# Kernel tuning notes

Measured on AMD Instinct MI355X. Metric: run time of the kernel, lower is better.

## Reference

```python
import jax, jax.numpy as jnp
import numpy as np

N, E, D, L, R, G, C = 50000, 800000, 64, 3, 2, 128, 10


def setup_inputs() -> dict:
    key = jax.random.key(0)
    ks = jax.random.split(key, 16)
    s = 0.05
    x = jax.random.normal(ks[0], (N, D), dtype=jnp.float32)
    edge_index = jax.random.randint(ks[1], (2, E), 0, N, dtype=jnp.int64)
    edge_type = jax.random.randint(ks[2], (E,), 0, R, dtype=jnp.int64)
    batch = jnp.sort(jax.random.randint(ks[3], (N,), 0, G, dtype=jnp.int64))
    # per-layer self-loop Linear, per-(layer,relation) GIN eps + 2-layer MLP
    self_W = jax.random.normal(ks[4], (L, D, D), dtype=jnp.float32) * s
    self_b = jax.random.normal(ks[5], (L, D), dtype=jnp.float32) * s
    eps = jnp.zeros((L, R), dtype=jnp.float32)  # eps=0, train_eps=True
    mlp_W1 = jax.random.normal(ks[6], (L, R, D, D), dtype=jnp.float32) * s
    mlp_b1 = jax.random.normal(ks[7], (L, R, D), dtype=jnp.float32) * s
    mlp_W2 = jax.random.normal(ks[8], (L, R, D, D), dtype=jnp.float32) * s
    mlp_b2 = jax.random.normal(ks[9], (L, R, D), dtype=jnp.float32) * s
    lin1_W = jax.random.normal(ks[10], (D, D), dtype=jnp.float32) * s
    lin1_b = jax.random.normal(ks[11], (D,), dtype=jnp.float32) * s
    lin2_W = jax.random.normal(ks[12], (D, C), dtype=jnp.float32) * s
    lin2_b = jax.random.normal(ks[13], (C,), dtype=jnp.float32) * s
    return {"x": x, "edge_index": edge_index, "edge_type": edge_type, "batch": batch,
            "self_W": self_W, "self_b": self_b, "eps": eps,
            "mlp_W1": mlp_W1, "mlp_b1": mlp_b1, "mlp_W2": mlp_W2, "mlp_b2": mlp_b2,
            "lin1_W": lin1_W, "lin1_b": lin1_b, "lin2_W": lin2_W, "lin2_b": lin2_b}


def reference(x, edge_index, edge_type, batch, self_W, self_b, eps,
              mlp_W1, mlp_b1, mlp_W2, mlp_b2, lin1_W, lin1_b, lin2_W, lin2_b):
    src, dst = edge_index[0], edge_index[1]
    h = x
    for l in range(L):
        x_new = h @ self_W[l] + self_b[l]
        x_src = h[src]  # [E, D] gather of source features, done once per layer
        for r in range(R):
            # per-relation edge masking + scatter-add aggregation
            msg = jnp.where((edge_type == r)[:, None], x_src, jnp.zeros((), h.dtype))
            agg = jax.ops.segment_sum(msg, dst, num_segments=N)  # [N, D]
            z = (1.0 + eps[l, r]) * h + agg  # GIN combine
            z = jax.nn.relu(z @ mlp_W1[l, r] + mlp_b1[l, r])
            x_new = x_new + (z @ mlp_W2[l, r] + mlp_b2[l, r])
        h = x_new
    # global mean pooling over graphs
    sums = jax.ops.segment_sum(h, batch, num_segments=G)  # [G, D]
    counts = jax.ops.segment_sum(jnp.ones((N,), h.dtype), batch, num_segments=G)
    pooled = sums / jnp.maximum(counts, 1.0)[:, None]
    out = jax.nn.relu(pooled @ lin1_W + lin1_b)
    # dropout omitted (eval mode)
    out = out @ lin2_W + lin2_b
    return out
```

## Files before the change

kernel.cpp:

```cpp
#include <hip/hip_runtime.h>

#define Nn 50000
#define Dd 64
#define Ee 800000
#define Ll 3
#define Rr 2
#define Gg 128
#define Cc 10
#define NR (Nn * Rr)
#define NB ((NR + 1023) / 1024)
#define NT (Nn / 16)

#define CVT_B  3125
#define PREP_B 240
#define HIST_B 3125

typedef __attribute__((ext_vector_type(8))) short short8;
typedef __attribute__((ext_vector_type(4))) float f32x4;

__device__ __forceinline__ unsigned short bf16_rne(float x) {
  unsigned u = __float_as_uint(x);
  unsigned r = u + 0x7fffu + ((u >> 16) & 1u);
  return (unsigned short)(r >> 16);
}
__device__ __forceinline__ float bf16_tof(unsigned short b) {
  return __uint_as_float(((unsigned)b) << 16);
}
__device__ __forceinline__ void acc8(float* z, uint4 u) {
  z[0] += __uint_as_float(u.x << 16);
  z[1] += __uint_as_float(u.x & 0xffff0000u);
  z[2] += __uint_as_float(u.y << 16);
  z[3] += __uint_as_float(u.y & 0xffff0000u);
  z[4] += __uint_as_float(u.z << 16);
  z[5] += __uint_as_float(u.z & 0xffff0000u);
  z[6] += __uint_as_float(u.w << 16);
  z[7] += __uint_as_float(u.w & 0xffff0000u);
}

__global__ __launch_bounds__(256) void k_setup(
    const float* __restrict__ x, unsigned short* __restrict__ hb,
    const float* __restrict__ selfW, const float* __restrict__ W1,
    const float* __restrict__ W2, unsigned short* __restrict__ wtHi,
    unsigned short* __restrict__ wtLo,
    const int* __restrict__ dst, const int* __restrict__ et,
    int* __restrict__ counts)
{
  int b = blockIdx.x;
  if (b < CVT_B) {
    int i = b * 256 + threadIdx.x;
    const float4 v = *(const float4*)&x[(size_t)i * 4];
    ushort4 o;
    o.x = bf16_rne(v.x); o.y = bf16_rne(v.y);
    o.z = bf16_rne(v.z); o.w = bf16_rne(v.w);
    *(ushort4*)&hb[(size_t)i * 4] = o;
  } else if (b < CVT_B + PREP_B) {
    int i = (b - CVT_B) * 256 + threadIdx.x;
    int l = i / (5 * 4096);
    int rem = i - l * 5 * 4096;
    int m = rem >> 12;
    int e = rem & 4095;
    int k = e >> 6, c = e & 63;
    const float* p;
    if (m == 0)      p = selfW + (size_t)l * 4096;
    else if (m == 1) p = W1 + ((size_t)l * 2 + 0) * 4096;
    else if (m == 2) p = W2 + ((size_t)l * 2 + 0) * 4096;
    else if (m == 3) p = W1 + ((size_t)l * 2 + 1) * 4096;
    else             p = W2 + ((size_t)l * 2 + 1) * 4096;
    float w = p[e];
    unsigned short hi = bf16_rne(w);
    unsigned short lo = bf16_rne(w - bf16_tof(hi));
    size_t o = ((size_t)(l * 5 + m) * 64 + c) * 64 + k;
    wtHi[o] = hi;
    wtLo[o] = lo;
  } else {
    int e = (b - CVT_B - PREP_B) * 256 + threadIdx.x;
    atomicAdd(&counts[et[e] * Nn + dst[e]], 1);
  }
}

__global__ __launch_bounds__(1024) void k_scan1(
    const int* __restrict__ counts, int* __restrict__ offs,
    int* __restrict__ btot)
{
  __shared__ int s[1024];
  int i = blockIdx.x * 1024 + threadIdx.x;
  int v = (i < NR) ? counts[i] : 0;
  s[threadIdx.x] = v;
  __syncthreads();
#pragma unroll
  for (int d = 1; d < 1024; d <<= 1) {
    int t = (threadIdx.x >= d) ? s[threadIdx.x - d] : 0;
    __syncthreads();
    s[threadIdx.x] += t;
    __syncthreads();
  }
  if (i < NR) offs[i + 1] = s[threadIdx.x];
  if (threadIdx.x == 1023) btot[blockIdx.x] = s[1023];
}

__global__ __launch_bounds__(128) void k_scan2(
    const int* __restrict__ btot, int* __restrict__ bscan)
{
  __shared__ int s[128];
  int v = (threadIdx.x < NB) ? btot[threadIdx.x] : 0;
  s[threadIdx.x] = v;
  __syncthreads();
#pragma unroll
  for (int d = 1; d < 128; d <<= 1) {
    int t = (threadIdx.x >= d) ? s[threadIdx.x - d] : 0;
    __syncthreads();
    s[threadIdx.x] += t;
    __syncthreads();
  }
  if (threadIdx.x < NB) bscan[threadIdx.x] = s[threadIdx.x] - v;
}

__global__ __launch_bounds__(1024) void k_scan3(
    const int* __restrict__ counts, const int* __restrict__ bscan,
    int* __restrict__ offs, int* __restrict__ cursor)
{
  int i = blockIdx.x * 1024 + threadIdx.x;
  if (i >= NR) return;
  int o = offs[i + 1] + bscan[blockIdx.x];
  offs[i + 1] = o;
  cursor[i] = o - counts[i];
  if (i == 0) offs[0] = 0;
}

__global__ __launch_bounds__(256) void k_fill(
    const int* __restrict__ src, const int* __restrict__ dst,
    const int* __restrict__ et, int* __restrict__ cursor,
    int* __restrict__ elist)
{
  int e = blockIdx.x * 256 + threadIdx.x;
  if (e >= Ee) return;
  int pos = atomicAdd(&cursor[et[e] * Nn + dst[e]], 1);
  elist[pos] = src[e];
}

#define WOFF(m, c, ks) ((size_t)(m)*4096 + (size_t)(c)*64 + (ks)*32 + koff)

__global__ __launch_bounds__(128, 8) void k_update(
    const float* __restrict__ h, const unsigned short* __restrict__ hb,
    const int* __restrict__ offs, const int* __restrict__ elist,
    const unsigned short* __restrict__ wtHi, const unsigned short* __restrict__ wtLo,
    const float* __restrict__ selfb, const float* __restrict__ eps,
    const float* __restrict__ b1, const float* __restrict__ b2,
    float* __restrict__ hn, unsigned short* __restrict__ hnb, int l)
{
  __shared__ __align__(16) unsigned short tbh[2][16 * 72];
  __shared__ __align__(16) unsigned short tbl[2][16 * 72];
  float* xfer = (float*)&tbh[0][0];
  const int wave = threadIdx.x >> 6;
  const int lane = threadIdx.x & 63;
  const int task = blockIdx.x;
  const int r = wave;
  const int idx15 = lane & 15;
  const int kg = lane >> 4;
  const int koff = kg * 8;
  const int nodeA = task * 16 + idx15;

  float f[2][8];
  {
    const float* hp = &h[(size_t)nodeA * 64 + koff];
    const float4 a0 = *(const float4*)(hp);
    const float4 a1 = *(const float4*)(hp + 4);
    const float4 b0 = *(const float4*)(hp + 32);
    const float4 b1v = *(const float4*)(hp + 36);
    f[0][0] = a0.x; f[0][1] = a0.y; f[0][2] = a0.z; f[0][3] = a0.w;
    f[0][4] = a1.x; f[0][5] = a1.y; f[0][6] = a1.z; f[0][7] = a1.w;
    f[1][0] = b0.x; f[1][1] = b0.y; f[1][2] = b0.z; f[1][3] = b0.w;
    f[1][4] = b1v.x; f[1][5] = b1v.y; f[1][6] = b1v.z; f[1][7] = b1v.w;
  }

  const unsigned short* whi = wtHi + (size_t)l * 5 * 4096;
  const unsigned short* wlo = wtLo + (size_t)l * 5 * 4096;
  const int m1 = 1 + 2 * r, m2 = 2 + 2 * r;
  const float er = 1.0f + eps[l * Rr + r];

  float za[2][8];
#pragma unroll
  for (int ks = 0; ks < 2; ++ks)
#pragma unroll
    for (int j = 0; j < 8; ++j) za[ks][j] = 0.0f;
  {
    int aidx = r * Nn + nodeA;
    int jb = offs[aidx], je = offs[aidx + 1];
    int j = jb;
    for (; j + 3 < je; j += 4) {
      int s0 = elist[j], s1 = elist[j + 1], s2 = elist[j + 2], s3 = elist[j + 3];
      const unsigned short* q0 = &hb[(size_t)s0 * 64 + koff];
      const unsigned short* q1 = &hb[(size_t)s1 * 64 + koff];
      const unsigned short* q2 = &hb[(size_t)s2 * 64 + koff];
      const unsigned short* q3 = &hb[(size_t)s3 * 64 + koff];
      const uint4 a0 = *(const uint4*)(q0);
      const uint4 a1 = *(const uint4*)(q1);
      const uint4 a2 = *(const uint4*)(q2);
      const uint4 a3 = *(const uint4*)(q3);
      const uint4 b0 = *(const uint4*)(q0 + 32);
      const uint4 b1q = *(const uint4*)(q1 + 32);
      const uint4 b2q = *(const uint4*)(q2 + 32);
      const uint4 b3 = *(const uint4*)(q3 + 32);
      acc8(za[0], a0); acc8(za[0], a1); acc8(za[0], a2); acc8(za[0], a3);
      acc8(za[1], b0); acc8(za[1], b1q); acc8(za[1], b2q); acc8(za[1], b3);
    }
    for (; j < je; ++j) {
      const unsigned short* q = &hb[(size_t)elist[j] * 64 + koff];
      const uint4 a = *(const uint4*)(q);
      const uint4 b = *(const uint4*)(q + 32);
      acc8(za[0], a); acc8(za[1], b);
    }
  }

  short8 zhi[2], zlo[2];
#pragma unroll
  for (int ks = 0; ks < 2; ++ks)
#pragma unroll
    for (int j = 0; j < 8; ++j) {
      float zf = er * f[ks][j] + za[ks][j];
      unsigned short hb2 = bf16_rne(zf);
      zhi[ks][j] = (short)hb2;
      zlo[ks][j] = (short)bf16_rne(zf - bf16_tof(hb2));
    }

  f32x4 tacc[4];
#pragma unroll
  for (int cb = 0; cb < 4; ++cb) {
    float bi = b1[((size_t)l * 2 + r) * 64 + cb * 16 + idx15];
    tacc[cb] = (f32x4){bi, bi, bi, bi};
  }
#pragma unroll
  for (int cb = 0; cb < 4; ++cb) {
    int c = cb * 16 + idx15;
#pragma unroll
    for (int ks = 0; ks < 2; ++ks) {
      const short8 bh = *(const short8*)&whi[WOFF(m1, c, ks)];
      const short8 bl = *(const short8*)&wlo[WOFF(m1, c, ks)];
      tacc[cb] = __builtin_amdgcn_mfma_f32_16x16x32_bf16(zhi[ks], bh, tacc[cb], 0, 0, 0);
      tacc[cb] = __builtin_amdgcn_mfma_f32_16x16x32_bf16(zhi[ks], bl, tacc[cb], 0, 0, 0);
      tacc[cb] = __builtin_amdgcn_mfma_f32_16x16x32_bf16(zlo[ks], bh, tacc[cb], 0, 0, 0);
    }
  }
#pragma unroll
  for (int cb = 0; cb < 4; ++cb)
#pragma unroll
    for (int q = 0; q < 4; ++q) {
      float tv = fmaxf(tacc[cb][q], 0.0f);
      unsigned short hb2 = bf16_rne(tv);
      tbh[wave][(kg * 4 + q) * 72 + cb * 16 + idx15] = hb2;
      tbl[wave][(kg * 4 + q) * 72 + cb * 16 + idx15] = bf16_rne(tv - bf16_tof(hb2));
    }
  asm volatile("s_waitcnt lgkmcnt(0)" ::: "memory");
  __builtin_amdgcn_sched_barrier(0);
  short8 thi[2], tlo[2];
#pragma unroll
  for (int ks = 0; ks < 2; ++ks) {
    thi[ks] = *(const short8*)&tbh[wave][idx15 * 72 + ks * 32 + koff];
    tlo[ks] = *(const short8*)&tbl[wave][idx15 * 72 + ks * 32 + koff];
  }

  f32x4 facc[4];
#pragma unroll
  for (int cb = 0; cb < 4; ++cb) {
    int c = cb * 16 + idx15;
    float bi = b2[((size_t)l * 2 + r) * 64 + c];
    if (wave == 1) bi += selfb[l * 64 + c];
    facc[cb] = (f32x4){bi, bi, bi, bi};
  }
#pragma unroll
  for (int cb = 0; cb < 4; ++cb) {
    int c = cb * 16 + idx15;
#pragma unroll
    for (int ks = 0; ks < 2; ++ks) {
      const short8 bh = *(const short8*)&whi[WOFF(m2, c, ks)];
      const short8 bl = *(const short8*)&wlo[WOFF(m2, c, ks)];
      facc[cb] = __builtin_amdgcn_mfma_f32_16x16x32_bf16(thi[ks], bh, facc[cb], 0, 0, 0);
      facc[cb] = __builtin_amdgcn_mfma_f32_16x16x32_bf16(thi[ks], bl, facc[cb], 0, 0, 0);
      facc[cb] = __builtin_amdgcn_mfma_f32_16x16x32_bf16(tlo[ks], bh, facc[cb], 0, 0, 0);
    }
  }
  if (wave == 1) {
    short8 ahi[2], alo[2];
#pragma unroll
    for (int ks = 0; ks < 2; ++ks)
#pragma unroll
      for (int j = 0; j < 8; ++j) {
        unsigned short hb2 = bf16_rne(f[ks][j]);
        ahi[ks][j] = (short)hb2;
        alo[ks][j] = (short)bf16_rne(f[ks][j] - bf16_tof(hb2));
      }
#pragma unroll
    for (int cb = 0; cb < 4; ++cb) {
      int c = cb * 16 + idx15;
#pragma unroll
      for (int ks = 0; ks < 2; ++ks) {
        const short8 bh = *(const short8*)&whi[WOFF(0, c, ks)];
        const short8 bl = *(const short8*)&wlo[WOFF(0, c, ks)];
        facc[cb] = __builtin_amdgcn_mfma_f32_16x16x32_bf16(ahi[ks], bh, facc[cb], 0, 0, 0);
        facc[cb] = __builtin_amdgcn_mfma_f32_16x16x32_bf16(ahi[ks], bl, facc[cb], 0, 0, 0);
        facc[cb] = __builtin_amdgcn_mfma_f32_16x16x32_bf16(alo[ks], bh, facc[cb], 0, 0, 0);
      }
    }
  }
  __syncthreads();
  if (wave == 1) {
#pragma unroll
    for (int cb = 0; cb < 4; ++cb)
#pragma unroll
      for (int q = 0; q < 4; ++q)
        xfer[(kg * 4 + q) * 65 + cb * 16 + idx15] = facc[cb][q];
  }
  __syncthreads();
  if (wave == 0) {
#pragma unroll
    for (int cb = 0; cb < 4; ++cb)
#pragma unroll
      for (int q = 0; q < 4; ++q) {
        int row = kg * 4 + q, col = cb * 16 + idx15;
        float v = facc[cb][q] + xfer[row * 65 + col];
        size_t o = ((size_t)task * 16 + row) * 64 + col;
        hn[o] = v;
        hnb[o] = bf16_rne(v);
      }
  }
}

__global__ __launch_bounds__(64) void k_poolhead(
    const float* __restrict__ h, const int* __restrict__ batch,
    const float* __restrict__ l1W, const float* __restrict__ l1b,
    const float* __restrict__ l2W, const float* __restrict__ l2b,
    float* __restrict__ out)
{
  int g = blockIdx.x;
  int lane = threadIdx.x;
  int lo = 0, hi = Nn;
  while (lo < hi) { int mid = (lo + hi) >> 1; if (batch[mid] < g) lo = mid + 1; else hi = mid; }
  int start = lo;
  hi = Nn;
  while (lo < hi) { int mid = (lo + hi) >> 1; if (batch[mid] < g + 1) lo = mid + 1; else hi = mid; }
  int end = lo;

  float acc = 0.0f;
  int i = start;
  for (; i + 3 < end; i += 4) {
    float v0 = h[(size_t)i * 64 + lane];
    float v1 = h[(size_t)(i + 1) * 64 + lane];
    float v2 = h[(size_t)(i + 2) * 64 + lane];
    float v3 = h[(size_t)(i + 3) * 64 + lane];
    acc += (v0 + v1) + (v2 + v3);
  }
  for (; i < end; ++i) acc += h[(size_t)i * 64 + lane];
  float p = acc / fmaxf((float)(end - start), 1.0f);

  float t = l1b[lane];
#pragma unroll
  for (int k = 0; k < Dd; ++k)
    t += __shfl(p, k, 64) * l1W[k * Dd + lane];
  t = fmaxf(t, 0.0f);
  float o = (lane < Cc) ? l2b[lane] : 0.0f;
#pragma unroll
  for (int k = 0; k < Dd; ++k) {
    float w = (lane < Cc) ? l2W[k * Cc + lane] : 0.0f;
    o += __shfl(t, k, 64) * w;
  }
  if (lane < Cc) out[(size_t)g * Cc + lane] = o;
}

extern "C" void kernel_launch(void* const* d_in, const int* in_sizes, int n_in,
                              void* d_out, int out_size, void* d_ws, size_t ws_size,
                              hipStream_t stream)
{
  const float* x     = (const float*)d_in[0];
  const int*   ei    = (const int*)d_in[1];
  const int*   et    = (const int*)d_in[2];
  const int*   batch = (const int*)d_in[3];
  const float* selfW = (const float*)d_in[4];
  const float* selfb = (const float*)d_in[5];
  const float* eps   = (const float*)d_in[6];
  const float* W1    = (const float*)d_in[7];
  const float* b1    = (const float*)d_in[8];
  const float* W2    = (const float*)d_in[9];
  const float* b2    = (const float*)d_in[10];
  const float* l1W   = (const float*)d_in[11];
  const float* l1b   = (const float*)d_in[12];
  const float* l2W   = (const float*)d_in[13];
  const float* l2b   = (const float*)d_in[14];
  float* out = (float*)d_out;

  float* buf0 = (float*)d_ws;
  float* buf1 = buf0 + (size_t)Nn * Dd;
  unsigned short* hb0 = (unsigned short*)(buf1 + (size_t)Nn * Dd);
  unsigned short* hb1 = hb0 + (size_t)Nn * Dd;
  unsigned short* wtHi = hb1 + (size_t)Nn * Dd;
  unsigned short* wtLo = wtHi + (size_t)Ll * 5 * 4096;
  int* counts = (int*)(wtLo + (size_t)Ll * 5 * 4096);
  int* offs   = counts + NR;
  int* cursor = offs + NR + 1;
  int* btot   = cursor + NR;
  int* bscan  = btot + NB;
  int* elist  = bscan + NB;

  const int* src = ei;
  const int* dst = ei + Ee;

  hipMemsetAsync(counts, 0, (size_t)NR * sizeof(int), stream);
  k_setup<<<CVT_B + PREP_B + HIST_B, 256, 0, stream>>>(
      x, hb0, selfW, W1, W2, wtHi, wtLo, dst, et, counts);

  k_scan1<<<NB, 1024, 0, stream>>>(counts, offs, btot);
  k_scan2<<<1, 128, 0, stream>>>(btot, bscan);
  k_scan3<<<NB, 1024, 0, stream>>>(counts, bscan, offs, cursor);
  k_fill<<<(Ee + 255) / 256, 256, 0, stream>>>(src, dst, et, cursor, elist);

  const float* h = x;
  const unsigned short* hbc = hb0;
  float* hn = buf0;
  unsigned short* hnb = hb1;
  for (int l = 0; l < Ll; ++l) {
    k_update<<<NT, 128, 0, stream>>>(h, hbc, offs, elist, wtHi, wtLo,
                                     selfb, eps, b1, b2, hn, hnb, l);
    h = hn;
    hbc = hnb;
    hn = (hn == buf0) ? buf1 : buf0;
    hnb = (hnb == hb0) ? hb1 : hb0;
  }
  k_poolhead<<<Gg, 64, 0, stream>>>(h, batch, l1W, l1b, l2W, l2b, out);
}
```

Before: 335.2 us.

## Sort nodes by total in-degree so update tiles share similar edge counts

Adds a counting sort of nodes by total in-degree (capped at 127), producing a permutation that the CSR scan, fill and update kernels use. Each 16-node MFMA tile then groups nodes with similar neighbour counts, which reduces lane divergence in the gather loop. Output rows are written back through the permutation, so stores become scattered rather than contiguous. The occupancy hint on the update kernel is also lowered from 8 to 5 blocks, and three small preprocessing launches are added.

Result: slower. 451.8 us (+34.8%).

```diff
diff --git a/kernel.cpp b/kernel.cpp
--- a/kernel.cpp
+++ b/kernel.cpp
@@ -78,13 +78,62 @@
   }
 }
 
+__global__ __launch_bounds__(256) void k_deghist(
+    const int* __restrict__ counts, int* __restrict__ binh)
+{
+  __shared__ int lh[128];
+  if (threadIdx.x < 128) lh[threadIdx.x] = 0;
+  __syncthreads();
+  int n = blockIdx.x * 256 + threadIdx.x;
+  if (n < Nn) {
+    int t = min(counts[n] + counts[Nn + n], 127);
+    atomicAdd(&lh[t], 1);
+  }
+  __syncthreads();
+  if (threadIdx.x < 128 && lh[threadIdx.x] > 0)
+    atomicAdd(&binh[threadIdx.x], lh[threadIdx.x]);
+}
+
+__global__ __launch_bounds__(128) void k_binscan(
+    const int* __restrict__ binh, int* __restrict__ bincur)
+{
+  __shared__ int s[128];
+  int v = binh[threadIdx.x];
+  s[threadIdx.x] = v;
+  __syncthreads();
+#pragma unroll
+  for (int d = 1; d < 128; d <<= 1) {
+    int t = (threadIdx.x >= d) ? s[threadIdx.x - d] : 0;
+    __syncthreads();
+    s[threadIdx.x] += t;
+    __syncthreads();
+  }
+  bincur[threadIdx.x] = s[threadIdx.x] - v;
+}
+
+__global__ __launch_bounds__(256) void k_scatterp(
+    const int* __restrict__ counts, int* __restrict__ bincur,
+    int* __restrict__ nodeof, int* __restrict__ permpos)
+{
+  int n = blockIdx.x * 256 + threadIdx.x;
+  if (n >= Nn) return;
+  int t = min(counts[n] + counts[Nn + n], 127);
+  int p = atomicAdd(&bincur[t], 1);
+  nodeof[p] = n;
+  permpos[n] = p;
+}
+
 __global__ __launch_bounds__(1024) void k_scan1(
-    const int* __restrict__ counts, int* __restrict__ offs,
-    int* __restrict__ btot)
+    const int* __restrict__ counts, const int* __restrict__ nodeof,
+    int* __restrict__ offs, int* __restrict__ btot)
 {
   __shared__ int s[1024];
   int i = blockIdx.x * 1024 + threadIdx.x;
-  int v = (i < NR) ? counts[i] : 0;
+  int v = 0;
+  if (i < NR) {
+    int rbase = (i >= Nn) ? Nn : 0;
+    v = counts[rbase + nodeof[i - rbase]];
+  }
   s[threadIdx.x] = v;
   __syncthreads();
 #pragma unroll
@@ -116,33 +165,36 @@
 }
 
 __global__ __launch_bounds__(1024) void k_scan3(
-    const int* __restrict__ counts, const int* __restrict__ bscan,
-    int* __restrict__ offs, int* __restrict__ cursor)
+    const int* __restrict__ counts, const int* __restrict__ nodeof,
+    const int* __restrict__ bscan, int* __restrict__ offs,
+    int* __restrict__ cursor)
 {
   int i = blockIdx.x * 1024 + threadIdx.x;
   if (i >= NR) return;
   int o = offs[i + 1] + bscan[blockIdx.x];
   offs[i + 1] = o;
-  cursor[i] = o - counts[i];
+  int rbase = (i >= Nn) ? Nn : 0;
+  cursor[i] = o - counts[rbase + nodeof[i - rbase]];
   if (i == 0) offs[0] = 0;
 }
 
 __global__ __launch_bounds__(256) void k_fill(
     const int* __restrict__ src, const int* __restrict__ dst,
-    const int* __restrict__ et, int* __restrict__ cursor,
-    int* __restrict__ elist)
+    const int* __restrict__ et, const int* __restrict__ permpos,
+    int* __restrict__ cursor, int* __restrict__ elist)
 {
   int e = blockIdx.x * 256 + threadIdx.x;
   if (e >= Ee) return;
-  int pos = atomicAdd(&cursor[et[e] * Nn + dst[e]], 1);
+  int pos = atomicAdd(&cursor[et[e] * Nn + permpos[dst[e]]], 1);
   elist[pos] = src[e];
 }
 
 #define WOFF(m, c, ks) ((size_t)(m)*4096 + (size_t)(c)*64 + (ks)*32 + koff)
 
-__global__ __launch_bounds__(128, 8) void k_update(
+__global__ __launch_bounds__(128, 5) void k_update(
     const float* __restrict__ h, const unsigned short* __restrict__ hb,
     const int* __restrict__ offs, const int* __restrict__ elist,
+    const int* __restrict__ nodeof,
     const unsigned short* __restrict__ wtHi, const unsigned short* __restrict__ wtLo,
     const float* __restrict__ selfb, const float* __restrict__ eps,
     const float* __restrict__ b1, const float* __restrict__ b2,
@@ -158,7 +210,8 @@
   const int idx15 = lane & 15;
   const int kg = lane >> 4;
   const int koff = kg * 8;
-  const int nodeA = task * 16 + idx15;
+  const int ppos = task * 16 + idx15;
+  const int nodeA = nodeof[ppos];
 
   float f[2][8];
   {
@@ -184,7 +237,7 @@
 #pragma unroll
     for (int j = 0; j < 8; ++j) za[ks][j] = 0.0f;
   {
-    int aidx = r * Nn + nodeA;
+    int aidx = r * Nn + ppos;
     int jb = offs[aidx], je = offs[aidx + 1];
     int j = jb;
     for (; j + 3 < je; j += 4) {
@@ -312,13 +365,16 @@
   }
   __syncthreads();
   if (wave == 0) {
+    int nrow[4];
+#pragma unroll
+    for (int q = 0; q < 4; ++q) nrow[q] = nodeof[task * 16 + kg * 4 + q];
 #pragma unroll
     for (int cb = 0; cb < 4; ++cb)
 #pragma unroll
       for (int q = 0; q < 4; ++q) {
         int row = kg * 4 + q, col = cb * 16 + idx15;
         float v = facc[cb][q] + xfer[row * 65 + col];
-        size_t o = ((size_t)task * 16 + row) * 64 + col;
+        size_t o = (size_t)nrow[q] * 64 + col;
         hn[o] = v;
         hnb[o] = bf16_rne(v);
       }
@@ -393,31 +449,38 @@
   unsigned short* hb1 = hb0 + (size_t)Nn * Dd;
   unsigned short* wtHi = hb1 + (size_t)Nn * Dd;
   unsigned short* wtLo = wtHi + (size_t)Ll * 5 * 4096;
-  int* counts = (int*)(wtLo + (size_t)Ll * 5 * 4096);
-  int* offs   = counts + NR;
-  int* cursor = offs + NR + 1;
-  int* btot   = cursor + NR;
-  int* bscan  = btot + NB;
-  int* elist  = bscan + NB;
+  int* counts  = (int*)(wtLo + (size_t)Ll * 5 * 4096);
+  int* binh    = counts + NR;
+  int* bincur  = binh + 128;
+  int* offs    = bincur + 128;
+  int* cursor  = offs + NR + 1;
+  int* btot    = cursor + NR;
+  int* bscan   = btot + NB;
+  int* elist   = bscan + NB;
+  int* nodeof  = elist + Ee;
+  int* permpos = nodeof + Nn;
 
   const int* src = ei;
   const int* dst = ei + Ee;
 
-  hipMemsetAsync(counts, 0, (size_t)NR * sizeof(int), stream);
+  hipMemsetAsync(counts, 0, (size_t)(NR + 256) * sizeof(int), stream);
   k_setup<<<CVT_B + PREP_B + HIST_B, 256, 0, stream>>>(
       x, hb0, selfW, W1, W2, wtHi, wtLo, dst, et, counts);
 
-  k_scan1<<<NB, 1024, 0, stream>>>(counts, offs, btot);
+  k_deghist<<<(Nn + 255) / 256, 256, 0, stream>>>(counts, binh);
+  k_binscan<<<1, 128, 0, stream>>>(binh, bincur);
+  k_scatterp<<<(Nn + 255) / 256, 256, 0, stream>>>(counts, bincur, nodeof, permpos);
+  k_scan1<<<NB, 1024, 0, stream>>>(counts, nodeof, offs, btot);
   k_scan2<<<1, 128, 0, stream>>>(btot, bscan);
-  k_scan3<<<NB, 1024, 0, stream>>>(counts, bscan, offs, cursor);
-  k_fill<<<(Ee + 255) / 256, 256, 0, stream>>>(src, dst, et, cursor, elist);
+  k_scan3<<<NB, 1024, 0, stream>>>(counts, nodeof, bscan, offs, cursor);
+  k_fill<<<(Ee + 255) / 256, 256, 0, stream>>>(src, dst, et, permpos, cursor, elist);
 
   const float* h = x;
   const unsigned short* hbc = hb0;
   float* hn = buf0;
   unsigned short* hnb = hb1;
   for (int l = 0; l < Ll; ++l) {
-    k_update<<<NT, 128, 0, stream>>>(h, hbc, offs, elist, wtHi, wtLo,
+    k_update<<<NT, 128, 0, stream>>>(h, hbc, offs, elist, nodeof, wtHi, wtLo,
                                      selfb, eps, b1, b2, hn, hnb, l);
     h = hn;
     hbc = hnb;
```
